# Kernel tuning notes

Measured on AMD Instinct MI355X. Metric: run time of the kernel, lower is better.

The kernel has to match this reference:

```python
import jax, jax.numpy as jnp
import numpy as np

B, S, D, H = 4, 2048, 512, 8
HD = D // H  # head_dim = 64


def setup_inputs() -> dict:
    key = jax.random.key(0)
    ks = jax.random.split(key, 16)
    sd = 1.0 / np.sqrt(D)
    def lin(ka, kb):
        W = jax.random.uniform(ka, (D, D), jnp.float32, -sd, sd)
        b = jax.random.uniform(kb, (D,), jnp.float32, -sd, sd)
        return W, b
    Wq, bq = lin(ks[0], ks[1])
    Wk, bk = lin(ks[2], ks[3])
    Wv, bv = lin(ks[4], ks[5])
    Wo, bo = lin(ks[6], ks[7])
    Ws, bs = lin(ks[8], ks[9])
    Wsh, bsh = lin(ks[10], ks[11])
    mod1_feat = jax.random.normal(ks[12], (B, S, D), jnp.float32)
    mod2_feat = jax.random.normal(ks[13], (B, S, D), jnp.float32)
    return {"mod1_feat": mod1_feat, "mod2_feat": mod2_feat,
            "Wq": Wq, "bq": bq, "Wk": Wk, "bk": bk, "Wv": Wv, "bv": bv,
            "Wo": Wo, "bo": bo, "Ws": Ws, "bs": bs, "Wsh": Wsh, "bsh": bsh}


def _heads(x):
    # [B, S, D] -> [B, H, S, HD]
    b, s, _ = x.shape
    return x.reshape(b, s, H, HD).transpose(0, 2, 1, 3)


def reference(mod1_feat, mod2_feat, Wq, bq, Wk, bk, Wv, bv, Wo, bo, Ws, bs, Wsh, bsh):
    Q = _heads(mod1_feat @ Wq + bq)
    K = _heads(mod2_feat @ Wk + bk)
    V = _heads(mod2_feat @ Wv + bv)
    scale = _heads(mod2_feat @ Ws + bs)
    shift = _heads(mod2_feat @ Wsh + bsh)
    K = K * scale + shift
    V = V * scale + shift
    scores = jnp.einsum('bhqd,bhkd->bhqk', Q, K) / jnp.sqrt(jnp.float32(HD))
    attn = jax.nn.softmax(scores, axis=-1)
    out = jnp.einsum('bhqk,bhkd->bhqd', attn, V)  # [B, H, S, HD]
    out = out.transpose(0, 2, 1, 3).reshape(mod1_feat.shape[0], -1, H * HD)
    return out @ Wo + bo
```

## Files before the change

kernel.cpp:

```cpp
#include <hip/hip_runtime.h>
#include <hip/hip_bf16.h>
#include <cstdint>
#include <cstddef>

typedef __bf16 bf16_t;
typedef __bf16 bf16x8 __attribute__((ext_vector_type(8)));
typedef __bf16 bf16x4 __attribute__((ext_vector_type(4)));
typedef float f32x4 __attribute__((ext_vector_type(4)));

#define DEVINL static __device__ __forceinline__

constexpr int B_ = 4, S_ = 2048, D_ = 512, H_ = 8, HD_ = 64;
constexpr int M_ = B_ * S_;
constexpr int NIN = 14;

DEVINL bf16x8 load8g(const bf16_t* p) { return *reinterpret_cast<const bf16x8*>(p); }

DEVINL int swcol(int col, int row) {
  return (col & ~63) | ((((col >> 3) ^ row) & 7) << 3) | (col & 7);
}

DEVINL int pK(int row) { return (row & 3) | (((row >> 3) & 1) << 2); }
DEVINL int swcolK(int col, int row) {
  return (col & ~63) | ((((col >> 3) ^ pK(row)) & 7) << 3) | (col & 7);
}

DEVINL void gl2lds(const bf16_t* g, bf16_t* l) {
  __builtin_amdgcn_global_load_lds(
      (const __attribute__((address_space(1))) void*)g,
      (__attribute__((address_space(3))) void*)l, 16, 0, 0);
}

DEVINL void stage16(bf16_t* dst, const void* src, size_t off, bool f32) {
  if (f32) {
    const float* p = (const float*)src + off;
    bf16x8 v0, v1;
#pragma unroll
    for (int j = 0; j < 8; ++j) { v0[j] = (bf16_t)p[j]; v1[j] = (bf16_t)p[8 + j]; }
    *reinterpret_cast<bf16x8*>(dst)     = v0;
    *reinterpret_cast<bf16x8*>(dst + 8) = v1;
  } else {
    const bf16_t* p = (const bf16_t*)src + off;
    *reinterpret_cast<bf16x8*>(dst)     = load8g(p);
    *reinterpret_cast<bf16x8*>(dst + 8) = load8g(p + 8);
  }
}

DEVINL float readf(const void* p, size_t i, bool f32) {
  return f32 ? ((const float*)p)[i] : (float)((const bf16_t*)p)[i];
}

struct DetectArgs { const uint16_t* p[NIN]; int n[NIN]; int* flags; };

__global__ __launch_bounds__(64) void detect_kernel(DetectArgs a) {
  const int z = blockIdx.x;
  const uint16_t* p = a.p[z];
  const int n = a.n[z];
  const int t = threadIdx.x;
  int cnt = 0;
  for (int i = t; i < n; i += 64) {
    const int e = (p[i] >> 7) & 0xFF;
    cnt += (e >= 200);
  }
#pragma unroll
  for (int off = 32; off > 0; off >>= 1) cnt += __shfl_down(cnt, off, 64);
  if (t == 0) a.flags[z] = (cnt > 16) ? 1 : 0;
}

struct CvtArgs { const void* src[2]; bf16_t* dst[2]; int idx[2]; const int* flags; };

__global__ __launch_bounds__(256) void cvt_kernel(CvtArgs a) {
  const int z = blockIdx.y;
  const bool f32 = a.flags[a.idx[z]] != 0;
  const size_t i = ((size_t)blockIdx.x * 256 + threadIdx.x) * 8;
  const int row = (int)(i >> 9);
  const int col = (int)(i & 511);
  bf16_t* dst = a.dst[z] + (size_t)row * 512 + swcol(col, row);
  if (f32) {
    const float* p = (const float*)a.src[z] + i;
    bf16x8 v;
#pragma unroll
    for (int j = 0; j < 8; ++j) v[j] = (bf16_t)p[j];
    *reinterpret_cast<bf16x8*>(dst) = v;
  } else {
    *reinterpret_cast<bf16x8*>(dst) = load8g((const bf16_t*)a.src[z] + i);
  }
}

struct TransArgs { const void* src[6]; int srcIdx[6]; bf16_t* dst[6]; const int* flags; };

__global__ __launch_bounds__(256) void transpose_kernel(TransArgs a) {
  __shared__ bf16_t tile[64][80];
  const int w = blockIdx.z;
  const void* src = a.src[w];
  const bool f32 = a.flags[a.srcIdx[w]] != 0;
  bf16_t* dst = a.dst[w];
  const int k0 = blockIdx.x * 64, n0 = blockIdx.y * 64;
  const int t = threadIdx.x;
  const int r = t >> 2, c0 = (t & 3) * 16;
  stage16(&tile[r][c0], src, (size_t)(k0 + r) * 512 + n0 + c0, f32);
  __syncthreads();
  const int orow = n0 + r;
  bf16_t* o = dst + (size_t)orow * 512;
#pragma unroll
  for (int half = 0; half < 2; ++half) {
    bf16x8 ov;
#pragma unroll
    for (int j = 0; j < 8; ++j) ov[j] = tile[c0 + half * 8 + j][r];
    *reinterpret_cast<bf16x8*>(o + swcol(k0 + c0 + half * 8, orow)) = ov;
  }
}

struct GemmBatch {
  const bf16_t* A[3];
  const bf16_t* Bt[3];
  const void* bias[3]; int bIdx[3];
  void* C[3];          int cIdx[3];
  const int* flags;
};

__global__ __launch_bounds__(512) void gemm_bt_kernel(GemmBatch args) {
  constexpr int K = 512, N = 512;
  __shared__ bf16_t As[3][128][64];
  __shared__ bf16_t Bs[3][64][64];
  const int z = blockIdx.z;
  const bf16_t* Ag  = args.A[z];
  const bf16_t* Btg = args.Bt[z];
  const int m0 = blockIdx.x * 128, n0 = blockIdx.y * 64;
  const int t = threadIdx.x, lane = t & 63, wave = t >> 6;
  const int l16 = lane & 15, quad = lane >> 4;
  const int wm = wave * 16;
  const int lr = lane >> 3, lc = (lane & 7) * 8;

  auto stage = [&](int slot, int k0) {
#pragma unroll
    for (int s = 0; s < 2; ++s) {
      const int r = wm + s * 8;
      gl2lds(Ag + (size_t)(m0 + r + lr) * K + k0 + lc, &As[slot][r][0]);
    }
    gl2lds(Btg + (size_t)(n0 + wave * 8 + lr) * K + k0 + lc, &Bs[slot][wave * 8][0]);
  };

  f32x4 acc[4] = {};

  stage(0, 0);
  stage(1, 64);

  constexpr int NT = K / 64;
  int cur = 0;
  for (int kt = 0; kt < NT - 1; ++kt) {
    asm volatile("s_waitcnt vmcnt(3)\n\ts_barrier" ::: "memory");
    __builtin_amdgcn_sched_barrier(0);
    if (kt + 2 < NT) {
      const int slot2 = cur == 0 ? 2 : cur - 1;
      stage(slot2, (kt + 2) * 64);
    }
#pragma unroll
    for (int ks = 0; ks < 2; ++ks) {
      const int sw = swcol(ks * 32 + quad * 8, l16);
      bf16x8 af = *reinterpret_cast<const bf16x8*>(&As[cur][wm + l16][sw]);
      bf16x8 bfr[4];
#pragma unroll
      for (int j = 0; j < 4; ++j)
        bfr[j] = *reinterpret_cast<const bf16x8*>(&Bs[cur][j * 16 + l16][sw]);
#pragma unroll
      for (int j = 0; j < 4; ++j)
        acc[j] = __builtin_amdgcn_mfma_f32_16x16x32_bf16(af, bfr[j], acc[j], 0, 0, 0);
    }
    cur = (cur == 2) ? 0 : cur + 1;
  }
  asm volatile("s_waitcnt vmcnt(0)\n\ts_barrier" ::: "memory");
  __builtin_amdgcn_sched_barrier(0);
#pragma unroll
  for (int ks = 0; ks < 2; ++ks) {
    const int sw = swcol(ks * 32 + quad * 8, l16);
    bf16x8 af = *reinterpret_cast<const bf16x8*>(&As[cur][wm + l16][sw]);
    bf16x8 bfr[4];
#pragma unroll
    for (int j = 0; j < 4; ++j)
      bfr[j] = *reinterpret_cast<const bf16x8*>(&Bs[cur][j * 16 + l16][sw]);
#pragma unroll
    for (int j = 0; j < 4; ++j)
      acc[j] = __builtin_amdgcn_mfma_f32_16x16x32_bf16(af, bfr[j], acc[j], 0, 0, 0);
  }

  const void* biag = args.bias[z];
  void* Cg         = args.C[z];
  const bool bf32 = args.bIdx[z] >= 0 && args.flags[args.bIdx[z]];
  const bool cf32 = args.cIdx[z] >= 0 && args.flags[args.cIdx[z]];
#pragma unroll
  for (int j = 0; j < 4; ++j) {
    const int col = n0 + j * 16 + l16;
    const float bv = readf(biag, col, bf32);
    const int rowb = m0 + wm + quad * 4;
#pragma unroll
    for (int r = 0; r < 4; ++r) {
      const size_t idx = (size_t)(rowb + r) * N + col;
      const float v = acc[j][r] + bv;
      if (cf32) ((float*)Cg)[idx] = v;
      else      ((bf16_t*)Cg)[idx] = (bf16_t)v;
    }
  }
}

struct KsvArgs {
  const bf16_t* A;
  const bf16_t* Bt[4];
  const void* bias[4]; int bIdx[4];
  bf16_t* Kmod;
  bf16_t* VtT;
  const int* flags;
};

__global__ __launch_bounds__(512) void ksv_kernel(KsvArgs args) {
  constexpr int K = 512;
  __shared__ bf16_t As[3][128][64];
  __shared__ bf16_t Bs[3][4][64][64];
  const int m0 = blockIdx.x * 128, n0 = blockIdx.y * 64;
  const int t = threadIdx.x, lane = t & 63, wave = t >> 6;
  const int l16 = lane & 15, quad = lane >> 4;
  const int wm = (wave >> 2) * 64;
  const int wn = (wave & 3) * 16;
  const int lr = lane >> 3, lc = (lane & 7) * 8;

  auto stage = [&](int slot, int k0) {
#pragma unroll
    for (int s = 0; s < 2; ++s) {
      const int r = wave * 16 + s * 8;
      gl2lds(args.A + (size_t)(m0 + r + lr) * K + k0 + lc, &As[slot][r][0]);
    }
    const int mat = wave >> 1;
    const int rb = (wave & 1) * 32;
#pragma unroll
    for (int s = 0; s < 4; ++s) {
      const int r = rb + s * 8;
      gl2lds(args.Bt[mat] + (size_t)(n0 + r + lr) * K + k0 + lc, &Bs[slot][mat][r][0]);
    }
  };

  f32x4 acc[4][4] = {};

  stage(0, 0);
  stage(1, 64);

  constexpr int NT = K / 64;
  int cur = 0;
  for (int kt = 0; kt < NT - 1; ++kt) {
    asm volatile("s_waitcnt vmcnt(6)\n\ts_barrier" ::: "memory");
    __builtin_amdgcn_sched_barrier(0);
    if (kt + 2 < NT) {
      const int slot2 = cur == 0 ? 2 : cur - 1;
      stage(slot2, (kt + 2) * 64);
    }
#pragma unroll
    for (int ks = 0; ks < 2; ++ks) {
      const int sw = swcol(ks * 32 + quad * 8, l16);
      bf16x8 af[4], bfr[4];
#pragma unroll
      for (int mi = 0; mi < 4; ++mi)
        af[mi] = *reinterpret_cast<const bf16x8*>(&As[cur][wm + mi * 16 + l16][sw]);
#pragma unroll
      for (int mat = 0; mat < 4; ++mat)
        bfr[mat] = *reinterpret_cast<const bf16x8*>(&Bs[cur][mat][wn + l16][sw]);
#pragma unroll
      for (int mat = 0; mat < 4; ++mat)
#pragma unroll
        for (int mi = 0; mi < 4; ++mi)
          acc[mat][mi] = __builtin_amdgcn_mfma_f32_16x16x32_bf16(af[mi], bfr[mat], acc[mat][mi], 0, 0, 0);
    }
    cur = (cur == 2) ? 0 : cur + 1;
  }
  asm volatile("s_waitcnt vmcnt(0)\n\ts_barrier" ::: "memory");
  __builtin_amdgcn_sched_barrier(0);
#pragma unroll
  for (int ks = 0; ks < 2; ++ks) {
    const int sw = swcol(ks * 32 + quad * 8, l16);
    bf16x8 af[4], bfr[4];
#pragma unroll
    for (int mi = 0; mi < 4; ++mi)
      af[mi] = *reinterpret_cast<const bf16x8*>(&As[cur][wm + mi * 16 + l16][sw]);
#pragma unroll
    for (int mat = 0; mat < 4; ++mat)
      bfr[mat] = *reinterpret_cast<const bf16x8*>(&Bs[cur][mat][wn + l16][sw]);
#pragma unroll
    for (int mat = 0; mat < 4; ++mat)
#pragma unroll
      for (int mi = 0; mi < 4; ++mi)
        acc[mat][mi] = __builtin_amdgcn_mfma_f32_16x16x32_bf16(af[mi], bfr[mat], acc[mat][mi], 0, 0, 0);
  }

  const int col = n0 + wn + l16;
  const float bk  = readf(args.bias[0], col, args.bIdx[0] >= 0 && args.flags[args.bIdx[0]]);
  const float bv  = readf(args.bias[1], col, args.bIdx[1] >= 0 && args.flags[args.bIdx[1]]);
  const float bs  = readf(args.bias[2], col, args.bIdx[2] >= 0 && args.flags[args.bIdx[2]]);
  const float bsh = readf(args.bias[3], col, args.bIdx[3] >= 0 && args.flags[args.bIdx[3]]);
  const int hh = col >> 6, dd = col & 63;
#pragma unroll
  for (int mi = 0; mi < 4; ++mi) {
    const int rowb = m0 + wm + mi * 16 + quad * 4;
    bf16x4 vpack;
#pragma unroll
    for (int r = 0; r < 4; ++r) {
      const int row = rowb + r;
      const float s  = acc[2][mi][r] + bs;
      const float sh = acc[3][mi][r] + bsh;
      const float kk = fmaf(acc[0][mi][r] + bk, s, sh);
      const float vv = fmaf(acc[1][mi][r] + bv, s, sh);
      args.Kmod[(size_t)row * 512 + swcolK(col, row)] = (bf16_t)kk;
      vpack[r] = (bf16_t)vv;
    }
    const int bb = rowb >> 11;
    const int ss = rowb & 2047;
    *reinterpret_cast<bf16x4*>(
        args.VtT + (((size_t)(bb * H_ + hh)) * HD_ + dd) * S_ + swcol(ss, dd)) = vpack;
  }
}

__global__ __launch_bounds__(512) void attn_kernel(const bf16_t* Q, const bf16_t* Kb,
                                                   const bf16_t* Vt, bf16_t* O) {
  __shared__ bf16_t Ks[3][64][64];
  __shared__ bf16_t Vs[3][64][64];
  const int i = blockIdx.x;
  const int xcd = i & 7, g = i >> 3;
  const int slice = xcd * 4 + (g & 3);
  const int qt = g >> 2;
  const int b = slice >> 3, h = slice & 7;
  const int t = threadIdx.x, wave = t >> 6, lane = t & 63;
  const int l16 = lane & 15, quad = lane >> 4;
  const int q0 = qt * 128 + wave * 16;
  const int lr = lane >> 3, lc = (lane & 7) * 8;

  bf16x8 ones;
#pragma unroll
  for (int j = 0; j < 8; ++j) ones[j] = (bf16_t)1.0f;

  bf16x8 qf[2];
  {
    const size_t qrow = ((size_t)b * S_ + q0 + l16) * D_ + h * HD_;
    qf[0] = load8g(Q + qrow + quad * 8);
    qf[1] = load8g(Q + qrow + 32 + quad * 8);
  }

  f32x4 oacc[4] = {};
  f32x4 lacc = {};

  const size_t kbase = (size_t)b * S_ * D_ + h * HD_;
  const size_t vbase = ((size_t)(b * H_ + h)) * HD_ * S_;

  const int rbase = ((l16 >> 2) << 3) | (l16 & 3);
  int koff[2][4];
#pragma unroll
  for (int j = 0; j < 4; ++j) {
    const int rho = rbase + (j >> 1) * 32 + (j & 1) * 4;
#pragma unroll
    for (int dc = 0; dc < 2; ++dc)
      koff[dc][j] = rho * 64 + swcolK(dc * 32 + quad * 8, rho);
  }
  const int voff[2] = { swcol(quad * 8, l16), swcol(32 + quad * 8, l16) };

  auto stage = [&](int slot, int k0) {
    const int r = wave * 8;
    gl2lds(Kb + kbase + (size_t)(k0 + r + lr) * D_ + lc, &Ks[slot][r][0]);
    gl2lds(Vt + vbase + (size_t)(r + lr) * S_ + k0 + lc, &Vs[slot][r][0]);
  };

  constexpr float CE = 0.18033688011112042f;

  auto compute = [&](int cur) {
    f32x4 sacc[4] = {};
    const bf16_t* ksbase = &Ks[cur][0][0];
#pragma unroll
    for (int dc = 0; dc < 2; ++dc) {
      bf16x8 kf[4];
#pragma unroll
      for (int j = 0; j < 4; ++j)
        kf[j] = *reinterpret_cast<const bf16x8*>(ksbase + koff[dc][j]);
#pragma unroll
      for (int j = 0; j < 4; ++j)
        sacc[j] = __builtin_amdgcn_mfma_f32_16x16x32_bf16(kf[j], qf[dc], sacc[j], 0, 0, 0);
    }
#pragma unroll
    for (int kc = 0; kc < 2; ++kc) {
      bf16x8 vf[4];
#pragma unroll
      for (int dj = 0; dj < 4; ++dj)
        vf[dj] = *reinterpret_cast<const bf16x8*>(&Vs[cur][dj * 16 + l16][voff[kc]]);
      bf16x8 bp;
#pragma unroll
      for (int r = 0; r < 4; ++r) {
        bp[r]     = (bf16_t)__builtin_amdgcn_exp2f(fminf(sacc[kc * 2][r]     * CE, 57.5f));
        bp[4 + r] = (bf16_t)__builtin_amdgcn_exp2f(fminf(sacc[kc * 2 + 1][r] * CE, 57.5f));
      }
#pragma unroll
      for (int dj = 0; dj < 4; ++dj)
        oacc[dj] = __builtin_amdgcn_mfma_f32_16x16x32_bf16(vf[dj], bp, oacc[dj], 0, 0, 0);
      lacc = __builtin_amdgcn_mfma_f32_16x16x32_bf16(ones, bp, lacc, 0, 0, 0);
    }
  };

  asm volatile("s_waitcnt vmcnt(0)" ::: "memory");
  stage(0, 0);
  stage(1, 64);

  constexpr int NT = S_ / 64;
  int cur = 0;
  for (int kt = 0; kt < NT - 1; ++kt) {
    asm volatile("s_waitcnt vmcnt(2)\n\ts_barrier" ::: "memory");
    __builtin_amdgcn_sched_barrier(0);
    if (kt + 2 < NT) {
      const int slot2 = cur == 0 ? 2 : cur - 1;
      stage(slot2, (kt + 2) * 64);
    }
    compute(cur);
    cur = (cur == 2) ? 0 : cur + 1;
  }
  asm volatile("s_waitcnt vmcnt(0)\n\ts_barrier" ::: "memory");
  __builtin_amdgcn_sched_barrier(0);
  compute(cur);

  {
    const float linv = 1.0f / fmaxf(lacc[0], 1e-30f);
    const int q = q0 + l16;
    const size_t orow = ((size_t)b * S_ + q) * D_ + h * HD_;
#pragma unroll
    for (int dj = 0; dj < 4; ++dj) {
      bf16x4 pack;
#pragma unroll
      for (int r = 0; r < 4; ++r) pack[r] = (bf16_t)(oacc[dj][r] * linv);
      *reinterpret_cast<bf16x4*>(&O[orow + swcol(dj * 16 + quad * 4, q)]) = pack;
    }
  }
}

extern "C" void kernel_launch(void* const* d_in, const int* in_sizes, int n_in,
                              void* d_out, int out_size, void* d_ws, size_t ws_size,
                              hipStream_t stream) {
  (void)n_in; (void)out_size; (void)ws_size;

  char* ws = (char*)d_ws;
  auto alloc = [&](size_t bytes) -> char* {
    char* p = ws; ws += (bytes + 255) & ~(size_t)255; return p;
  };
  int* flags = (int*)alloc(64 * sizeof(int));
  const size_t wbytes = (size_t)512 * 512 * sizeof(bf16_t);
  const size_t fbytes = (size_t)M_ * D_ * sizeof(bf16_t);
  bf16_t* wt    = (bf16_t*)alloc(6 * wbytes);
  bf16_t* m1b   = (bf16_t*)alloc(fbytes);
  bf16_t* m2b   = (bf16_t*)alloc(fbytes);
  bf16_t* q_buf = (bf16_t*)alloc(fbytes);
  bf16_t* atmp  = (bf16_t*)alloc(fbytes);
  bf16_t* kmod  = (bf16_t*)alloc(fbytes);
  bf16_t* vtb    = m1b;
  bf16_t* attn_b = atmp;

  bf16_t* wtq  = wt + 0 * 512 * 512;
  bf16_t* wtk  = wt + 1 * 512 * 512;
  bf16_t* wtv  = wt + 2 * 512 * 512;
  bf16_t* wts  = wt + 3 * 512 * 512;
  bf16_t* wtsh = wt + 4 * 512 * 512;
  bf16_t* wto  = wt + 5 * 512 * 512;

  DetectArgs da;
  for (int i = 0; i < NIN; ++i) {
    da.p[i] = (const uint16_t*)d_in[i];
    da.n[i] = in_sizes[i] < 2048 ? in_sizes[i] : 2048;
  }
  da.flags = flags;
  hipLaunchKernelGGL(detect_kernel, dim3(NIN), dim3(64), 0, stream, da);

  CvtArgs ca;
  ca.src[0] = d_in[0]; ca.dst[0] = m1b; ca.idx[0] = 0;
  ca.src[1] = d_in[1]; ca.dst[1] = m2b; ca.idx[1] = 1;
  ca.flags = flags;
  hipLaunchKernelGGL(cvt_kernel, dim3(M_ * D_ / 2048, 2), dim3(256), 0, stream, ca);

  TransArgs ta;
  const int widx[6] = {2, 4, 6, 10, 12, 8};
  bf16_t* wdst[6] = {wtq, wtk, wtv, wts, wtsh, wto};
  for (int i = 0; i < 6; ++i) { ta.src[i] = d_in[widx[i]]; ta.srcIdx[i] = widx[i]; ta.dst[i] = wdst[i]; }
  ta.flags = flags;
  hipLaunchKernelGGL(transpose_kernel, dim3(8, 8, 6), dim3(256), 0, stream, ta);

  GemmBatch g1;
  g1.A[0] = m1b;  g1.A[1] = m1b;  g1.A[2] = m1b;
  g1.Bt[0] = wtq; g1.Bt[1] = wtq; g1.Bt[2] = wtq;
  g1.bias[0] = d_in[3];  g1.bIdx[0] = 3;
  g1.bias[1] = d_in[3];  g1.bIdx[1] = 3;
  g1.bias[2] = d_in[3];  g1.bIdx[2] = 3;
  g1.C[0] = q_buf; g1.cIdx[0] = -1;
  g1.C[1] = q_buf; g1.cIdx[1] = -1;
  g1.C[2] = q_buf; g1.cIdx[2] = -1;
  g1.flags = flags;
  hipLaunchKernelGGL(gemm_bt_kernel, dim3(M_ / 128, 8, 1), dim3(512), 0, stream, g1);

  KsvArgs kv;
  kv.A = m2b;
  kv.Bt[0] = wtk; kv.Bt[1] = wtv; kv.Bt[2] = wts; kv.Bt[3] = wtsh;
  kv.bias[0] = d_in[5];  kv.bIdx[0] = 5;
  kv.bias[1] = d_in[7];  kv.bIdx[1] = 7;
  kv.bias[2] = d_in[11]; kv.bIdx[2] = 11;
  kv.bias[3] = d_in[13]; kv.bIdx[3] = 13;
  kv.Kmod = kmod; kv.VtT = vtb;
  kv.flags = flags;
  hipLaunchKernelGGL(ksv_kernel, dim3(M_ / 128, 8), dim3(512), 0, stream, kv);

  hipLaunchKernelGGL(attn_kernel, dim3(512), dim3(512), 0, stream,
                     q_buf, kmod, vtb, attn_b);

  GemmBatch g2;
  for (int i = 0; i < 3; ++i) {
    g2.A[i] = attn_b;
    g2.Bt[i] = wto;
    g2.bias[i] = d_in[9]; g2.bIdx[i] = 9;
    g2.C[i] = d_out; g2.cIdx[i] = 0;
  }
  g2.flags = flags;
  hipLaunchKernelGGL(gemm_bt_kernel, dim3(M_ / 128, 8, 1), dim3(512), 0, stream, g2);
}
```

Baseline: 201.8 us.

## Merge convert and transpose prep kernels; split KSV GEMM across 16 waves

Merges the input bf16 conversion and the weight transpose into one prep kernel, dispatching on block index, so one launch replaces two. The fused K/V/scale/shift GEMM now runs 1024 threads per block. Each wave computes 32 rows instead of 64, which halves its accumulators and loads per stage and adjusts the vmcnt wait to match. This aims for more latency hiding and less register pressure per wave, at the cost of fewer blocks per CU and the same LDS footprint.

```diff
diff --git a/kernel.cpp b/kernel.cpp
--- a/kernel.cpp
+++ b/kernel.cpp
@@ -67,47 +67,53 @@
   if (t == 0) a.flags[z] = (cnt > 16) ? 1 : 0;
 }
 
-struct CvtArgs { const void* src[2]; bf16_t* dst[2]; int idx[2]; const int* flags; };
-
-__global__ __launch_bounds__(256) void cvt_kernel(CvtArgs a) {
-  const int z = blockIdx.y;
-  const bool f32 = a.flags[a.idx[z]] != 0;
-  const size_t i = ((size_t)blockIdx.x * 256 + threadIdx.x) * 8;
-  const int row = (int)(i >> 9);
-  const int col = (int)(i & 511);
-  bf16_t* dst = a.dst[z] + (size_t)row * 512 + swcol(col, row);
-  if (f32) {
-    const float* p = (const float*)a.src[z] + i;
-    bf16x8 v;
-#pragma unroll
-    for (int j = 0; j < 8; ++j) v[j] = (bf16_t)p[j];
-    *reinterpret_cast<bf16x8*>(dst) = v;
+struct PrepArgs {
+  const void* csrc[2]; bf16_t* cdst[2]; int cidx[2];
+  const void* wsrc[6]; int wIdx[6]; bf16_t* wdst[6];
+  const int* flags;
+};
+
+__global__ __launch_bounds__(256) void prep_kernel(PrepArgs a) {
+  __shared__ bf16_t tile[64][80];
+  const int bid = blockIdx.x;
+  if (bid < 4096) {
+    const int z = bid >> 11;
+    const int bx = bid & 2047;
+    const bool f32 = a.flags[a.cidx[z]] != 0;
+    const size_t i = ((size_t)bx * 256 + threadIdx.x) * 8;
+    const int row = (int)(i >> 9);
+    const int col = (int)(i & 511);
+    bf16_t* dst = a.cdst[z] + (size_t)row * 512 + swcol(col, row);
+    if (f32) {
+      const float* p = (const float*)a.csrc[z] + i;
+      bf16x8 v;
+#pragma unroll
+      for (int j = 0; j < 8; ++j) v[j] = (bf16_t)p[j];
+      *reinterpret_cast<bf16x8*>(dst) = v;
+    } else {
+      *reinterpret_cast<bf16x8*>(dst) = load8g((const bf16_t*)a.csrc[z] + i);
+    }
   } else {
-    *reinterpret_cast<bf16x8*>(dst) = load8g((const bf16_t*)a.src[z] + i);
-  }
-}
-
-struct TransArgs { const void* src[6]; int srcIdx[6]; bf16_t* dst[6]; const int* flags; };
-
-__global__ __launch_bounds__(256) void transpose_kernel(TransArgs a) {
-  __shared__ bf16_t tile[64][80];
-  const int w = blockIdx.z;
-  const void* src = a.src[w];
-  const bool f32 = a.flags[a.srcIdx[w]] != 0;
-  bf16_t* dst = a.dst[w];
-  const int k0 = blockIdx.x * 64, n0 = blockIdx.y * 64;
-  const int t = threadIdx.x;
-  const int r = t >> 2, c0 = (t & 3) * 16;
-  stage16(&tile[r][c0], src, (size_t)(k0 + r) * 512 + n0 + c0, f32);
-  __syncthreads();
-  const int orow = n0 + r;
-  bf16_t* o = dst + (size_t)orow * 512;
-#pragma unroll
-  for (int half = 0; half < 2; ++half) {
-    bf16x8 ov;
-#pragma unroll
-    for (int j = 0; j < 8; ++j) ov[j] = tile[c0 + half * 8 + j][r];
-    *reinterpret_cast<bf16x8*>(o + swcol(k0 + c0 + half * 8, orow)) = ov;
+    const int rem = bid - 4096;
+    const int w = rem >> 6;
+    const int r6 = rem & 63;
+    const int k0 = (r6 & 7) * 64, n0 = (r6 >> 3) * 64;
+    const void* src = a.wsrc[w];
+    const bool f32 = a.flags[a.wIdx[w]] != 0;
+    bf16_t* dst = a.wdst[w];
+    const int t = threadIdx.x;
+    const int r = t >> 2, c0 = (t & 3) * 16;
+    stage16(&tile[r][c0], src, (size_t)(k0 + r) * 512 + n0 + c0, f32);
+    __syncthreads();
+    const int orow = n0 + r;
+    bf16_t* o = dst + (size_t)orow * 512;
+#pragma unroll
+    for (int half = 0; half < 2; ++half) {
+      bf16x8 ov;
+#pragma unroll
+      for (int j = 0; j < 8; ++j) ov[j] = tile[c0 + half * 8 + j][r];
+      *reinterpret_cast<bf16x8*>(o + swcol(k0 + c0 + half * 8, orow)) = ov;
+    }
   }
 }
 
@@ -212,33 +218,29 @@
   const int* flags;
 };
 
-__global__ __launch_bounds__(512) void ksv_kernel(KsvArgs args) {
+__global__ __launch_bounds__(1024) void ksv_kernel(KsvArgs args) {
   constexpr int K = 512;
   __shared__ bf16_t As[3][128][64];
   __shared__ bf16_t Bs[3][4][64][64];
   const int m0 = blockIdx.x * 128, n0 = blockIdx.y * 64;
   const int t = threadIdx.x, lane = t & 63, wave = t >> 6;
   const int l16 = lane & 15, quad = lane >> 4;
-  const int wm = (wave >> 2) * 64;
+  const int wm = (wave >> 2) * 32;
   const int wn = (wave & 3) * 16;
   const int lr = lane >> 3, lc = (lane & 7) * 8;
 
   auto stage = [&](int slot, int k0) {
+    gl2lds(args.A + (size_t)(m0 + wave * 8 + lr) * K + k0 + lc, &As[slot][wave * 8][0]);
+    const int mat = wave >> 2;
+    const int rb = (wave & 3) * 16;
 #pragma unroll
     for (int s = 0; s < 2; ++s) {
-      const int r = wave * 16 + s * 8;
-      gl2lds(args.A + (size_t)(m0 + r + lr) * K + k0 + lc, &As[slot][r][0]);
-    }
-    const int mat = wave >> 1;
-    const int rb = (wave & 1) * 32;
-#pragma unroll
-    for (int s = 0; s < 4; ++s) {
       const int r = rb + s * 8;
       gl2lds(args.Bt[mat] + (size_t)(n0 + r + lr) * K + k0 + lc, &Bs[slot][mat][r][0]);
     }
   };
 
-  f32x4 acc[4][4] = {};
+  f32x4 acc[4][2] = {};
 
   stage(0, 0);
   stage(1, 64);
@@ -246,7 +248,7 @@
   constexpr int NT = K / 64;
   int cur = 0;
   for (int kt = 0; kt < NT - 1; ++kt) {
-    asm volatile("s_waitcnt vmcnt(6)\n\ts_barrier" ::: "memory");
+    asm volatile("s_waitcnt vmcnt(3)\n\ts_barrier" ::: "memory");
     __builtin_amdgcn_sched_barrier(0);
     if (kt + 2 < NT) {
       const int slot2 = cur == 0 ? 2 : cur - 1;
@@ -255,9 +257,9 @@
 #pragma unroll
     for (int ks = 0; ks < 2; ++ks) {
       const int sw = swcol(ks * 32 + quad * 8, l16);
-      bf16x8 af[4], bfr[4];
-#pragma unroll
-      for (int mi = 0; mi < 4; ++mi)
+      bf16x8 af[2], bfr[4];
+#pragma unroll
+      for (int mi = 0; mi < 2; ++mi)
         af[mi] = *reinterpret_cast<const bf16x8*>(&As[cur][wm + mi * 16 + l16][sw]);
 #pragma unroll
       for (int mat = 0; mat < 4; ++mat)
@@ -265,7 +267,7 @@
 #pragma unroll
       for (int mat = 0; mat < 4; ++mat)
 #pragma unroll
-        for (int mi = 0; mi < 4; ++mi)
+        for (int mi = 0; mi < 2; ++mi)
           acc[mat][mi] = __builtin_amdgcn_mfma_f32_16x16x32_bf16(af[mi], bfr[mat], acc[mat][mi], 0, 0, 0);
     }
     cur = (cur == 2) ? 0 : cur + 1;
@@ -275,9 +277,9 @@
 #pragma unroll
   for (int ks = 0; ks < 2; ++ks) {
     const int sw = swcol(ks * 32 + quad * 8, l16);
-    bf16x8 af[4], bfr[4];
-#pragma unroll
-    for (int mi = 0; mi < 4; ++mi)
+    bf16x8 af[2], bfr[4];
+#pragma unroll
+    for (int mi = 0; mi < 2; ++mi)
       af[mi] = *reinterpret_cast<const bf16x8*>(&As[cur][wm + mi * 16 + l16][sw]);
 #pragma unroll
     for (int mat = 0; mat < 4; ++mat)
@@ -285,7 +287,7 @@
 #pragma unroll
     for (int mat = 0; mat < 4; ++mat)
 #pragma unroll
-      for (int mi = 0; mi < 4; ++mi)
+      for (int mi = 0; mi < 2; ++mi)
         acc[mat][mi] = __builtin_amdgcn_mfma_f32_16x16x32_bf16(af[mi], bfr[mat], acc[mat][mi], 0, 0, 0);
   }
 
@@ -296,7 +298,7 @@
   const float bsh = readf(args.bias[3], col, args.bIdx[3] >= 0 && args.flags[args.bIdx[3]]);
   const int hh = col >> 6, dd = col & 63;
 #pragma unroll
-  for (int mi = 0; mi < 4; ++mi) {
+  for (int mi = 0; mi < 2; ++mi) {
     const int rowb = m0 + wm + mi * 16 + quad * 4;
     bf16x4 vpack;
 #pragma unroll
@@ -468,18 +470,14 @@
   da.flags = flags;
   hipLaunchKernelGGL(detect_kernel, dim3(NIN), dim3(64), 0, stream, da);
 
-  CvtArgs ca;
-  ca.src[0] = d_in[0]; ca.dst[0] = m1b; ca.idx[0] = 0;
-  ca.src[1] = d_in[1]; ca.dst[1] = m2b; ca.idx[1] = 1;
-  ca.flags = flags;
-  hipLaunchKernelGGL(cvt_kernel, dim3(M_ * D_ / 2048, 2), dim3(256), 0, stream, ca);
-
-  TransArgs ta;
+  PrepArgs pa;
+  pa.csrc[0] = d_in[0]; pa.cdst[0] = m1b; pa.cidx[0] = 0;
+  pa.csrc[1] = d_in[1]; pa.cdst[1] = m2b; pa.cidx[1] = 1;
   const int widx[6] = {2, 4, 6, 10, 12, 8};
   bf16_t* wdst[6] = {wtq, wtk, wtv, wts, wtsh, wto};
-  for (int i = 0; i < 6; ++i) { ta.src[i] = d_in[widx[i]]; ta.srcIdx[i] = widx[i]; ta.dst[i] = wdst[i]; }
-  ta.flags = flags;
-  hipLaunchKernelGGL(transpose_kernel, dim3(8, 8, 6), dim3(256), 0, stream, ta);
+  for (int i = 0; i < 6; ++i) { pa.wsrc[i] = d_in[widx[i]]; pa.wIdx[i] = widx[i]; pa.wdst[i] = wdst[i]; }
+  pa.flags = flags;
+  hipLaunchKernelGGL(prep_kernel, dim3(4096 + 384), dim3(256), 0, stream, pa);
 
   GemmBatch g1;
   g1.A[0] = m1b;  g1.A[1] = m1b;  g1.A[2] = m1b;
@@ -502,7 +500,7 @@
   kv.bias[3] = d_in[13]; kv.bIdx[3] = 13;
   kv.Kmod = kmod; kv.VtT = vtb;
   kv.flags = flags;
-  hipLaunchKernelGGL(ksv_kernel, dim3(M_ / 128, 8), dim3(512), 0, stream, kv);
+  hipLaunchKernelGGL(ksv_kernel, dim3(M_ / 128, 8), dim3(1024), 0, stream, kv);
 
   hipLaunchKernelGGL(attn_kernel, dim3(512), dim3(512), 0, stream,
                      q_buf, kmod, vtb, attn_b);
```

Measured after the change: 194.8 us. -3.5%, faster.
